# Kernel optimization log

Measured on AMD Instinct MI355X. Metric: run time of the kernel, lower is better.

The kernel has to match this reference:

```python
import jax, jax.numpy as jnp
import numpy as np
import math

B, T, D = 2, 2048, 2048
N_HEADS, N_KV, HEAD_DIM = 16, 4, 128
INTER = 8192
MAX_POS = 4096
ROPE_BASE = 10000.0
EPS = 1e-6


def _rope_tables():
    inv_freq = 1.0 / (ROPE_BASE ** (jnp.arange(0, HEAD_DIM, 2, dtype=jnp.float32) / HEAD_DIM))
    t = jnp.arange(MAX_POS, dtype=jnp.float32)
    freqs = jnp.einsum('i,j->ij', t, inv_freq)          # [MAX_POS, HEAD_DIM//2]
    emb = jnp.concatenate([freqs, freqs], axis=-1)      # [MAX_POS, HEAD_DIM]
    return jnp.cos(emb), jnp.sin(emb)


def _apply_rope(x, cos, sin):
    # x: [B,H,T,Dh]; cos/sin: [B,T,Dh] (gathered by position_ids)
    c = cos[:, None, :, :]
    s = sin[:, None, :, :]
    x1 = x[..., ::2]
    x2 = x[..., 1::2]
    x_rot = jnp.stack([-x2, x1], axis=-1).reshape(x.shape)  # interleave(-x2, x1)
    return x * c + x_rot * s


def _rms_norm(x, w):
    var = jnp.mean(x * x, axis=-1, keepdims=True)
    return w * (x * jax.lax.rsqrt(var + EPS))


def setup_inputs() -> dict:
    key = jax.random.key(0)
    ks = jax.random.split(key, 10)
    s = 0.02
    hidden_states = jax.random.normal(ks[0], (B, T, D), dtype=jnp.float32)
    # additive causal mask
    causal = jnp.tril(jnp.ones((T, T), dtype=bool))
    attention_mask = jnp.where(causal, 0.0, -1e9).astype(jnp.float32)[None, None]
    position_ids = jnp.arange(B * T).reshape(B, T)  # values < MAX_POS
    return {
        'hidden_states': hidden_states,
        'attention_mask': attention_mask,
        'position_ids': position_ids,
        'attn_norm_w': jnp.ones((D,), jnp.float32),
        'mlp_norm_w': jnp.ones((D,), jnp.float32),
        'wq': jax.random.normal(ks[1], (D, N_HEADS * HEAD_DIM), jnp.float32) * s,
        'wk': jax.random.normal(ks[2], (D, N_KV * HEAD_DIM), jnp.float32) * s,
        'wv': jax.random.normal(ks[3], (D, N_KV * HEAD_DIM), jnp.float32) * s,
        'wo': jax.random.normal(ks[4], (N_HEADS * HEAD_DIM, D), jnp.float32) * s,
        'gate_w': jax.random.normal(ks[5], (D, D), jnp.float32) * s,
        'gate_b': jnp.zeros((D,), jnp.float32),
        'fc1_w': jax.random.normal(ks[6], (D, INTER), jnp.float32) * s,
        'fc2_w': jax.random.normal(ks[7], (INTER, D), jnp.float32) * s,
    }


def reference(hidden_states, attention_mask, position_ids, attn_norm_w, mlp_norm_w,
              wq, wk, wv, wo, gate_w, gate_b, fc1_w, fc2_w):
    b, t, _ = hidden_states.shape
    residual = hidden_states
    h = _rms_norm(hidden_states, attn_norm_w)

    # elementwise sigmoid output gate: [B,T,D] -> [B,H,T,Dh]
    gate = jax.nn.sigmoid(h @ gate_w + gate_b)
    gate = gate.reshape(b, t, N_HEADS, HEAD_DIM).transpose(0, 2, 1, 3)

    q = (h @ wq).reshape(b, t, N_HEADS, HEAD_DIM).transpose(0, 2, 1, 3)
    k = (h @ wk).reshape(b, t, N_KV, HEAD_DIM).transpose(0, 2, 1, 3)
    v = (h @ wv).reshape(b, t, N_KV, HEAD_DIM).transpose(0, 2, 1, 3)

    cos_t, sin_t = _rope_tables()
    cos = cos_t[position_ids]  # [B,T,Dh]
    sin = sin_t[position_ids]
    q = _apply_rope(q, cos, sin)
    k = _apply_rope(k, cos, sin)

    n_rep = N_HEADS // N_KV
    k = jnp.repeat(k, n_rep, axis=1)  # GQA expand to [B,H,T,Dh]
    v = jnp.repeat(v, n_rep, axis=1)

    scores = jnp.einsum('bhqd,bhkd->bhqk', q, k) / math.sqrt(HEAD_DIM)
    scores = scores + attention_mask
    attn = jax.nn.softmax(scores, axis=-1)
    out = jnp.einsum('bhqk,bhkd->bhqd', attn, v) * gate
    out = out.transpose(0, 2, 1, 3).reshape(b, t, N_HEADS * HEAD_DIM) @ wo

    h = residual + out
    residual = h
    h2 = _rms_norm(h, mlp_norm_w)
    mlp_out = jax.nn.silu(h2 @ fc1_w) @ fc2_w
    return residual + mlp_out
```

## Files before the change

kernel.cpp:

```cpp
#include <hip/hip_runtime.h>
#include <hip/hip_bf16.h>
#include <cstdint>
#include <cstddef>

#define BB 2
#define TT 2048
#define DD 2048
#define NH 16
#define NKV 4
#define HD 128
#define NI 8192
#define MM (BB*TT)

typedef __bf16 bf16x8 __attribute__((ext_vector_type(8)));
typedef float  f32x4  __attribute__((ext_vector_type(4)));

__device__ __forceinline__ void gload_lds16(const void* g, void* l) {
  __builtin_amdgcn_global_load_lds((__attribute__((address_space(1))) void*)g,
                                   (__attribute__((address_space(3))) void*)l,
                                   16, 0, 0);
}

__device__ __forceinline__ int xcd_swizzle(int wg, int nwg) {
  int xcd = wg & 7;
  int l = wg >> 3;
  int q = nwg >> 3, r = nwg & 7;
  return (xcd < r ? xcd * (q + 1) : r * (q + 1) + (xcd - r) * q) + l;
}

__global__ __launch_bounds__(128) void rope_tables_k(float* __restrict__ cosT,
                                                     float* __restrict__ sinT) {
  int pos = blockIdx.x;
  int d = threadIdx.x;
  int f = d & 63;
  float inv = powf(10000.0f, -((float)(2 * f)) / 128.0f);
  float ang = inv * (float)pos;
  cosT[pos * 128 + d] = cosf(ang);
  sinT[pos * 128 + d] = sinf(ang);
}

template <typename TIN>
__global__ __launch_bounds__(256) void transpose_to_bf16_k(const TIN* __restrict__ in,
                                                           __bf16* __restrict__ out,
                                                           int R, int C) {
  __shared__ float t[32][33];
  int c0 = blockIdx.x * 32, r0 = blockIdx.y * 32;
  int tx = threadIdx.x & 31;
  int ty = threadIdx.x >> 5;
#pragma unroll
  for (int i = 0; i < 4; i++) {
    int r = ty + i * 8;
    t[r][tx] = (float)in[(size_t)(r0 + r) * C + c0 + tx];
  }
  __syncthreads();
#pragma unroll
  for (int i = 0; i < 4; i++) {
    int r = ty + i * 8;
    out[(size_t)(c0 + r) * R + r0 + tx] = (__bf16)t[tx][r];
  }
}

__global__ __launch_bounds__(256) void rmsnorm_k(const float* __restrict__ x,
                                                 const float* __restrict__ w,
                                                 __bf16* __restrict__ out) {
  int row = blockIdx.x;
  const float* xr = x + (size_t)row * DD;
  int t = threadIdx.x;
  float4 a = ((const float4*)xr)[2 * t];
  float4 b = ((const float4*)xr)[2 * t + 1];
  float ss = a.x * a.x + a.y * a.y + a.z * a.z + a.w * a.w +
             b.x * b.x + b.y * b.y + b.z * b.z + b.w * b.w;
#pragma unroll
  for (int off = 32; off; off >>= 1) ss += __shfl_xor(ss, off, 64);
  __shared__ float red[4];
  if ((t & 63) == 0) red[t >> 6] = ss;
  __syncthreads();
  float tot = red[0] + red[1] + red[2] + red[3];
  float rs = rsqrtf(tot * (1.0f / DD) + 1e-6f);
  const float4 w1 = ((const float4*)w)[2 * t];
  const float4 w2 = ((const float4*)w)[2 * t + 1];
  bf16x8 ov;
  ov[0] = (__bf16)(a.x * rs * w1.x);
  ov[1] = (__bf16)(a.y * rs * w1.y);
  ov[2] = (__bf16)(a.z * rs * w1.z);
  ov[3] = (__bf16)(a.w * rs * w1.w);
  ov[4] = (__bf16)(b.x * rs * w2.x);
  ov[5] = (__bf16)(b.y * rs * w2.y);
  ov[6] = (__bf16)(b.z * rs * w2.z);
  ov[7] = (__bf16)(b.w * rs * w2.w);
  *(bf16x8*)(out + (size_t)row * DD + t * 8) = ov;
}

enum { EPI_BF16 = 0, EPI_ROPE = 1, EPI_SIG = 2, EPI_RES = 3, EPI_SILU = 4 };

template <int EPI>
__global__ __launch_bounds__(256) void gemm_k(
    const __bf16* __restrict__ A, const __bf16* __restrict__ Bt,
    __bf16* __restrict__ outB, float* __restrict__ outF,
    const float* __restrict__ bias, const float* __restrict__ residual,
    const float* __restrict__ cosT, const float* __restrict__ sinT,
    const int* __restrict__ posids, int N, int K, float oscale) {
  __shared__ __align__(16) __bf16 As[128 * 32];
  __shared__ __align__(16) __bf16 Bs[128 * 32];
  const int tid = threadIdx.x;
  const int lane = tid & 63;
  const int w = tid >> 6;
  const int wm = w >> 1, wn = w & 1;

  const int nwg = gridDim.x * gridDim.y;
  int wg = xcd_swizzle(blockIdx.y * gridDim.x + blockIdx.x, nwg);
  const int bx = wg % gridDim.x, by = wg / gridDim.x;
  const int m0 = by * 128;
  const int n0 = bx * 128;

  const int lr = lane >> 2;
  const int lc = (lane & 3) * 8;
  const __bf16* aSrc = A + (size_t)(m0 + 32 * w + lr) * K + lc;
  const __bf16* bSrc = Bt + (size_t)(n0 + 32 * w + lr) * K + lc;
  __bf16* aDst = &As[w * 1024];
  __bf16* bDst = &Bs[w * 1024];

  f32x4 acc[4][4];
#pragma unroll
  for (int i = 0; i < 4; i++)
#pragma unroll
    for (int j = 0; j < 4; j++) acc[i][j] = (f32x4){0.f, 0.f, 0.f, 0.f};

  const int fr = lane & 15;
  const int fc = (lane >> 4) * 8;

  for (int k0 = 0; k0 < K; k0 += 32) {
    __syncthreads();
    gload_lds16(aSrc + k0, aDst);
    gload_lds16(aSrc + k0 + (size_t)16 * K, aDst + 512);
    gload_lds16(bSrc + k0, bDst);
    gload_lds16(bSrc + k0 + (size_t)16 * K, bDst + 512);
    asm volatile("s_waitcnt vmcnt(0)" ::: "memory");
    __syncthreads();

    bf16x8 af[4], bfg[4];
#pragma unroll
    for (int i = 0; i < 4; i++)
      af[i] = *(const bf16x8*)&As[(wm * 64 + i * 16 + fr) * 32 + fc];
#pragma unroll
    for (int i = 0; i < 4; i++)
      bfg[i] = *(const bf16x8*)&Bs[(wn * 64 + i * 16 + fr) * 32 + fc];
#pragma unroll
    for (int mi = 0; mi < 4; mi++)
#pragma unroll
      for (int ni = 0; ni < 4; ni++)
        acc[mi][ni] =
            __builtin_amdgcn_mfma_f32_16x16x32_bf16(af[mi], bfg[ni], acc[mi][ni], 0, 0, 0);
  }

  const int fg = lane >> 4;
#pragma unroll
  for (int mi = 0; mi < 4; mi++) {
#pragma unroll
    for (int ni = 0; ni < 4; ni++) {
#pragma unroll
      for (int j = 0; j < 4; j++) {
        int row = m0 + wm * 64 + mi * 16 + fg * 4 + j;
        int col = n0 + wn * 64 + ni * 16 + fr;
        float v = acc[mi][ni][j];
        if constexpr (EPI == EPI_BF16) {
          outB[(size_t)row * N + col] = (__bf16)v;
        } else if constexpr (EPI == EPI_ROPE) {
          float vp = __shfl_xor(v, 1, 64);
          int pos = posids[row];
          int d = col & 127;
          float c = cosT[pos * 128 + d];
          float s = sinT[pos * 128 + d];
          float o = (col & 1) ? (v * c + vp * s) : (v * c - vp * s);
          outB[(size_t)row * N + col] = (__bf16)(o * oscale);
        } else if constexpr (EPI == EPI_SIG) {
          float xx = v + bias[col];
          outB[(size_t)row * N + col] = (__bf16)(1.0f / (1.0f + expf(-xx)));
        } else if constexpr (EPI == EPI_RES) {
          outF[(size_t)row * N + col] = v + residual[(size_t)row * N + col];
        } else if constexpr (EPI == EPI_SILU) {
          outB[(size_t)row * N + col] = (__bf16)(v / (1.0f + expf(-v)));
        }
      }
    }
  }
}

__global__ __launch_bounds__(256) void attn_k(const __bf16* __restrict__ Q,
                                              const __bf16* __restrict__ Kb,
                                              const __bf16* __restrict__ Vt,
                                              const __bf16* __restrict__ Gate,
                                              __bf16* __restrict__ Out) {
  __shared__ __align__(16) __bf16 Ks[2][64 * 128];
  __shared__ __align__(16) __bf16 Vs[2][128 * 64];
  __shared__ __align__(16) __bf16 Ps[4][16 * 64];
  const int tid = threadIdx.x;
  const int lane = tid & 63;
  const int w = tid >> 6;
  const int fr = lane & 15;
  const int fg = lane >> 4;

  const int nwg = gridDim.x * gridDim.y;
  int wg = xcd_swizzle(blockIdx.y * gridDim.x + blockIdx.x, nwg);
  const int qb = wg % gridDim.x;
  const int bh = wg / gridDim.x;
  const int q0 = qb * 64;
  const int b = bh >> 4, h = bh & 15;
  const int g = h >> 2;

  const size_t qrow = (size_t)(b * TT + q0 + w * 16 + fr);
  bf16x8 qf[4];
#pragma unroll
  for (int kt = 0; kt < 4; kt++)
    qf[kt] = *(const bf16x8*)&Q[qrow * 2048 + h * 128 + kt * 32 + fg * 8];

  const __bf16* kPtr[4];
  const __bf16* vPtr[4];
#pragma unroll
  for (int i = 0; i < 4; i++) {
    int krow = w * 16 + i * 4 + (lane >> 4);
    int kcol8 = (lane & 15) ^ (krow & 15);
    kPtr[i] = Kb + (size_t)(b * TT + krow) * 512 + g * 128 + kcol8 * 8;
    int dloc = w * 32 + i * 8 + (lane >> 3);
    int kv8 = (lane & 7) ^ (dloc & 7);
    vPtr[i] = Vt + (size_t)(g * 128 + dloc) * (size_t)MM + b * TT + kv8 * 8;
  }

  f32x4 o[8];
#pragma unroll
  for (int i = 0; i < 8; i++) o[i] = (f32x4){0.f, 0.f, 0.f, 0.f};
  float mrow[4] = {-3e38f, -3e38f, -3e38f, -3e38f};
  float lrow[4] = {0.f, 0.f, 0.f, 0.f};

  const int nsteps = qb + 1;

#pragma unroll
  for (int i = 0; i < 4; i++) {
    gload_lds16(kPtr[i], &Ks[0][w * 2048 + i * 512]);
    gload_lds16(vPtr[i], &Vs[0][w * 2048 + i * 512]);
  }
  __syncthreads();

  for (int t = 0; t < nsteps; t++) {
    const int cur = t & 1;
    const int kb = t * 64;
    if (t + 1 < nsteps) {
      const int nb = kb + 64;
#pragma unroll
      for (int i = 0; i < 4; i++) {
        gload_lds16(kPtr[i] + (size_t)nb * 512, &Ks[cur ^ 1][w * 2048 + i * 512]);
        gload_lds16(vPtr[i] + nb, &Vs[cur ^ 1][w * 2048 + i * 512]);
      }
    }

    f32x4 s[4];
#pragma unroll
    for (int nc = 0; nc < 4; nc++) s[nc] = (f32x4){0.f, 0.f, 0.f, 0.f};
#pragma unroll
    for (int nc = 0; nc < 4; nc++)
#pragma unroll
      for (int kt = 0; kt < 4; kt++) {
        bf16x8 kf = *(const bf16x8*)&Ks[cur][(nc * 16 + fr) * 128 + (((kt * 4 + fg) ^ fr) << 3)];
        s[nc] = __builtin_amdgcn_mfma_f32_16x16x32_bf16(qf[kt], kf, s[nc], 0, 0, 0);
      }

    float alpha[4];
#pragma unroll
    for (int j = 0; j < 4; j++) {
      const int qr = q0 + w * 16 + fg * 4 + j;
      float pv[4];
#pragma unroll
      for (int nc = 0; nc < 4; nc++) {
        int kc = kb + nc * 16 + fr;
        float val = s[nc][j];
        if (kc > qr) val = -1e9f;
        pv[nc] = val;
      }
      float tmx = fmaxf(fmaxf(pv[0], pv[1]), fmaxf(pv[2], pv[3]));
      tmx = fmaxf(tmx, __shfl_xor(tmx, 1, 64));
      tmx = fmaxf(tmx, __shfl_xor(tmx, 2, 64));
      tmx = fmaxf(tmx, __shfl_xor(tmx, 4, 64));
      tmx = fmaxf(tmx, __shfl_xor(tmx, 8, 64));
      float mnew = fmaxf(mrow[j], tmx);
      alpha[j] = __expf(mrow[j] - mnew);
      mrow[j] = mnew;
      float rsum = 0.f;
      const int q = fg * 4 + j;
#pragma unroll
      for (int nc = 0; nc < 4; nc++) {
        float e = __expf(pv[nc] - mnew);
        rsum += e;
        Ps[w][q * 64 + (((nc * 2 + (fr >> 3)) ^ (q & 7)) << 3) + (fr & 7)] = (__bf16)e;
      }
      rsum += __shfl_xor(rsum, 1, 64);
      rsum += __shfl_xor(rsum, 2, 64);
      rsum += __shfl_xor(rsum, 4, 64);
      rsum += __shfl_xor(rsum, 8, 64);
      lrow[j] = lrow[j] * alpha[j] + rsum;
    }
#pragma unroll
    for (int nd = 0; nd < 8; nd++)
#pragma unroll
      for (int j = 0; j < 4; j++) o[nd][j] *= alpha[j];

    bf16x8 pa[2];
#pragma unroll
    for (int sl = 0; sl < 2; sl++)
      pa[sl] = *(const bf16x8*)&Ps[w][fr * 64 + (((sl * 4 + fg) ^ (fr & 7)) << 3)];
#pragma unroll
    for (int nd = 0; nd < 8; nd++)
#pragma unroll
      for (int sl = 0; sl < 2; sl++) {
        bf16x8 vf =
            *(const bf16x8*)&Vs[cur][(nd * 16 + fr) * 64 + (((sl * 4 + fg) ^ (fr & 7)) << 3)];
        o[nd] = __builtin_amdgcn_mfma_f32_16x16x32_bf16(pa[sl], vf, o[nd], 0, 0, 0);
      }
    __syncthreads();
  }

  float invl[4];
#pragma unroll
  for (int j = 0; j < 4; j++) invl[j] = 1.0f / lrow[j];
#pragma unroll
  for (int nd = 0; nd < 8; nd++) {
#pragma unroll
    for (int j = 0; j < 4; j++) {
      int row = q0 + w * 16 + fg * 4 + j;
      int d = nd * 16 + fr;
      size_t idx = (size_t)(b * TT + row) * 2048 + h * 128 + d;
      float val = o[nd][j] * invl[j] * (float)Gate[idx];
      Out[idx] = (__bf16)val;
    }
  }
}

extern "C" void kernel_launch(void* const* d_in, const int* in_sizes, int n_in,
                              void* d_out, int out_size, void* d_ws, size_t ws_size,
                              hipStream_t stream) {
  const float* hidden = (const float*)d_in[0];
  const int* posids = (const int*)d_in[2];
  const float* attn_w = (const float*)d_in[3];
  const float* mlp_w = (const float*)d_in[4];
  const float* wq = (const float*)d_in[5];
  const float* wk = (const float*)d_in[6];
  const float* wv = (const float*)d_in[7];
  const float* wo = (const float*)d_in[8];
  const float* gw = (const float*)d_in[9];
  const float* gb = (const float*)d_in[10];
  const float* f1 = (const float*)d_in[11];
  const float* f2 = (const float*)d_in[12];

  char* p = (char*)d_ws;
  auto alloc = [&](size_t n) {
    char* r = p;
    p += (n + 255) & ~(size_t)255;
    return r;
  };
  __bf16* wq_t = (__bf16*)alloc((size_t)2048 * 2048 * 2);
  __bf16* wk_t = (__bf16*)alloc((size_t)512 * 2048 * 2);
  __bf16* wv_t = (__bf16*)alloc((size_t)512 * 2048 * 2);
  __bf16* gw_t = (__bf16*)alloc((size_t)2048 * 2048 * 2);
  __bf16* wo_t = (__bf16*)alloc((size_t)2048 * 2048 * 2);
  __bf16* f1_t = (__bf16*)alloc((size_t)NI * 2048 * 2);
  __bf16* f2_t = (__bf16*)alloc((size_t)2048 * NI * 2);
  __bf16* h_bf = (__bf16*)alloc((size_t)MM * DD * 2);
  float* h1 = (float*)alloc((size_t)MM * 2048 * 4);

  char* regionA = alloc((size_t)64 * 1024 * 1024);
  __bf16* q_bf    = (__bf16*)(regionA);
  __bf16* gate_bf = (__bf16*)(regionA + (size_t)16 * 1024 * 1024);
  __bf16* attn_g  = (__bf16*)(regionA + (size_t)32 * 1024 * 1024);
  __bf16* k_bf    = (__bf16*)(regionA + (size_t)48 * 1024 * 1024);
  __bf16* v_bf    = (__bf16*)(regionA + (size_t)52 * 1024 * 1024);
  __bf16* v_t     = (__bf16*)(regionA + (size_t)56 * 1024 * 1024);
  float*  cosT    = (float*)(regionA + (size_t)60 * 1024 * 1024);
  float*  sinT    = (float*)(regionA + (size_t)62 * 1024 * 1024);
  __bf16* mlp1    = (__bf16*)(regionA);

  rope_tables_k<<<4096, 128, 0, stream>>>(cosT, sinT);

  transpose_to_bf16_k<float><<<dim3(2048 / 32, 2048 / 32), 256, 0, stream>>>(wq, wq_t, 2048, 2048);
  transpose_to_bf16_k<float><<<dim3(512 / 32, 2048 / 32), 256, 0, stream>>>(wk, wk_t, 2048, 512);
  transpose_to_bf16_k<float><<<dim3(512 / 32, 2048 / 32), 256, 0, stream>>>(wv, wv_t, 2048, 512);
  transpose_to_bf16_k<float><<<dim3(2048 / 32, 2048 / 32), 256, 0, stream>>>(gw, gw_t, 2048, 2048);
  transpose_to_bf16_k<float><<<dim3(2048 / 32, 2048 / 32), 256, 0, stream>>>(wo, wo_t, 2048, 2048);
  transpose_to_bf16_k<float><<<dim3(NI / 32, 2048 / 32), 256, 0, stream>>>(f1, f1_t, 2048, NI);
  transpose_to_bf16_k<float><<<dim3(2048 / 32, NI / 32), 256, 0, stream>>>(f2, f2_t, NI, 2048);

  rmsnorm_k<<<MM, 256, 0, stream>>>(hidden, attn_w, h_bf);

  const float qsc = 0.08838834764831845f;
  gemm_k<EPI_ROPE><<<dim3(16, 32), 256, 0, stream>>>(h_bf, wq_t, q_bf, nullptr, nullptr,
                                                     nullptr, cosT, sinT, posids, 2048, 2048, qsc);
  gemm_k<EPI_ROPE><<<dim3(4, 32), 256, 0, stream>>>(h_bf, wk_t, k_bf, nullptr, nullptr,
                                                    nullptr, cosT, sinT, posids, 512, 2048, 1.0f);
  gemm_k<EPI_BF16><<<dim3(4, 32), 256, 0, stream>>>(h_bf, wv_t, v_bf, nullptr, nullptr,
                                                    nullptr, nullptr, nullptr, nullptr, 512, 2048, 1.0f);
  gemm_k<EPI_SIG><<<dim3(16, 32), 256, 0, stream>>>(h_bf, gw_t, gate_bf, nullptr, gb,
                                                    nullptr, nullptr, nullptr, nullptr, 2048, 2048, 1.0f);

  transpose_to_bf16_k<__bf16><<<dim3(512 / 32, MM / 32), 256, 0, stream>>>(v_bf, v_t, MM, 512);

  attn_k<<<dim3(TT / 64, BB * NH), 256, 0, stream>>>(q_bf, k_bf, v_t, gate_bf, attn_g);

  gemm_k<EPI_RES><<<dim3(16, 32), 256, 0, stream>>>(attn_g, wo_t, nullptr, h1, nullptr,
                                                    hidden, nullptr, nullptr, nullptr, 2048, 2048, 1.0f);

  rmsnorm_k<<<MM, 256, 0, stream>>>(h1, mlp_w, h_bf);

  gemm_k<EPI_SILU><<<dim3(NI / 128, 32), 256, 0, stream>>>(h_bf, f1_t, mlp1, nullptr, nullptr,
                                                           nullptr, nullptr, nullptr, nullptr, NI, 2048, 1.0f);

  gemm_k<EPI_RES><<<dim3(16, 32), 256, 0, stream>>>(mlp1, f2_t, nullptr, (float*)d_out, nullptr,
                                                    h1, nullptr, nullptr, nullptr, 2048, NI, 1.0f);
}
```

Measured before the change: 904.3 us.

## Use 256x256 triple-buffered GEMM, fuse Q/gate and K/V projections, split-K fc2

Replaces the 128x128 GEMM with a 256x256-tile, 512-thread kernel. It uses three-stage LDS buffering with async global-to-LDS loads, XOR-swizzled LDS layout and raised priority around the MFMA block. The Q and gate weights are concatenated into one GEMM, and K and V into another, so each launch shares the same activation loads. The fc2 GEMM is split into two K halves, written as bf16 partials into the reused f1 weight buffer and summed with the residual in a combine kernel. This is meant to raise arithmetic intensity and cut launch count. In exchange it adds bf16 rounding of the partial sums and a larger LDS and register footprint that can lower occupancy.

Result: no change. 904.3 us (+0.0%).

```diff
diff --git a/kernel.cpp b/kernel.cpp
--- a/kernel.cpp
+++ b/kernel.cpp
@@ -91,15 +91,158 @@
   *(bf16x8*)(out + (size_t)row * DD + t * 8) = ov;
 }
 
-enum { EPI_BF16 = 0, EPI_ROPE = 1, EPI_SIG = 2, EPI_RES = 3, EPI_SILU = 4 };
+enum { G_QG = 0, G_RES = 1, G_SILU = 2, G_PART = 3 };
 
 template <int EPI>
-__global__ __launch_bounds__(256) void gemm_k(
+__global__ __launch_bounds__(512) void gemm256_k(
     const __bf16* __restrict__ A, const __bf16* __restrict__ Bt,
     __bf16* __restrict__ outB, float* __restrict__ outF,
+    __bf16* __restrict__ outQ, __bf16* __restrict__ outG,
     const float* __restrict__ bias, const float* __restrict__ residual,
     const float* __restrict__ cosT, const float* __restrict__ sinT,
-    const int* __restrict__ posids, int N, int K, float oscale) {
+    const int* __restrict__ posids, int N, int K, int ldk, float oscale) {
+  __shared__ __align__(16) __bf16 Ab[3][256 * 32];
+  __shared__ __align__(16) __bf16 Bb[3][256 * 32];
+  const int tid = threadIdx.x;
+  const int lane = tid & 63;
+  const int wid = tid >> 6;
+  const int wr = wid >> 2;
+  const int wc = wid & 3;
+  const int fr = lane & 15;
+  const int fg = lane >> 4;
+
+  const int nwg = gridDim.x * gridDim.y;
+  int wg = xcd_swizzle(blockIdx.y * gridDim.x + blockIdx.x, nwg);
+  const int bx = wg % gridDim.x, by = wg / gridDim.x;
+  const int m0 = by * 256;
+  const int n0 = bx * 256;
+  const int kz = blockIdx.z;
+  const int kBase = kz * K;
+
+  const int srow0 = wid * 32 + (lane >> 2);
+  const int scol = (((lane & 3) ^ ((lane >> 3) & 3)) << 3);
+  const __bf16* aS0 = A + (size_t)(m0 + srow0) * ldk + kBase + scol;
+  const __bf16* aS1 = aS0 + (size_t)16 * ldk;
+  const __bf16* bS0 = Bt + (size_t)(n0 + srow0) * ldk + kBase + scol;
+  const __bf16* bS1 = bS0 + (size_t)16 * ldk;
+  const int e0 = (wid * 2) * 512;
+  const int e1 = (wid * 2 + 1) * 512;
+
+  const int nt = K / 32;
+
+#define STAGE256(kt, s)                             \
+  {                                                 \
+    const int k0_ = (kt) * 32;                      \
+    gload_lds16(aS0 + k0_, &Ab[(s)][e0]);           \
+    gload_lds16(aS1 + k0_, &Ab[(s)][e1]);           \
+    gload_lds16(bS0 + k0_, &Bb[(s)][e0]);           \
+    gload_lds16(bS1 + k0_, &Bb[(s)][e1]);           \
+  }
+
+  STAGE256(0, 0);
+  if (nt > 1) STAGE256(1, 1);
+  asm volatile("s_waitcnt vmcnt(4)" ::: "memory");
+  __builtin_amdgcn_s_barrier();
+  __builtin_amdgcn_sched_barrier(0);
+
+  f32x4 acc[8][4];
+#pragma unroll
+  for (int i = 0; i < 8; i++)
+#pragma unroll
+    for (int j = 0; j < 4; j++) acc[i][j] = (f32x4){0.f, 0.f, 0.f, 0.f};
+
+  const int asl = (fg ^ ((fr >> 1) & 3)) * 8;
+
+  for (int t = 0; t < nt; ++t) {
+    const int s = t % 3;
+    if (t + 2 < nt) STAGE256(t + 2, (t + 2) % 3);
+    bf16x8 af[8], bfr[4];
+#pragma unroll
+    for (int mi = 0; mi < 8; mi++)
+      af[mi] = *(const bf16x8*)&Ab[s][(wr * 128 + mi * 16 + fr) * 32 + asl];
+#pragma unroll
+    for (int ni = 0; ni < 4; ni++)
+      bfr[ni] = *(const bf16x8*)&Bb[s][(wc * 64 + ni * 16 + fr) * 32 + asl];
+    __builtin_amdgcn_s_setprio(1);
+#pragma unroll
+    for (int mi = 0; mi < 8; mi++)
+#pragma unroll
+      for (int ni = 0; ni < 4; ni++)
+        acc[mi][ni] =
+            __builtin_amdgcn_mfma_f32_16x16x32_bf16(af[mi], bfr[ni], acc[mi][ni], 0, 0, 0);
+    __builtin_amdgcn_s_setprio(0);
+    if (t + 1 < nt) {
+      if (t + 2 < nt) {
+        asm volatile("s_waitcnt vmcnt(4)" ::: "memory");
+      } else {
+        asm volatile("s_waitcnt vmcnt(0)" ::: "memory");
+      }
+      __builtin_amdgcn_s_barrier();
+      __builtin_amdgcn_sched_barrier(0);
+    }
+  }
+#undef STAGE256
+
+#pragma unroll
+  for (int mi = 0; mi < 8; mi++) {
+    const int row = m0 + wr * 128 + mi * 16 + fg * 4;
+#pragma unroll
+    for (int ni = 0; ni < 4; ni++) {
+      const int col = n0 + wc * 64 + ni * 16 + fr;
+#pragma unroll
+      for (int j = 0; j < 4; j++) {
+        float v = acc[mi][ni][j];
+        const int r = row + j;
+        if constexpr (EPI == G_QG) {
+          float vp = __shfl_xor(v, 1, 64);
+          if (n0 < 2048) {
+            int pos = posids[r];
+            int d = col & 127;
+            float c = cosT[pos * 128 + d], sn = sinT[pos * 128 + d];
+            float o = (col & 1) ? (v * c + vp * sn) : (v * c - vp * sn);
+            outQ[(size_t)r * 2048 + col] = (__bf16)(o * oscale);
+          } else {
+            float xx = v + bias[col - 2048];
+            outG[(size_t)r * 2048 + (col - 2048)] = (__bf16)(1.0f / (1.0f + expf(-xx)));
+          }
+        } else if constexpr (EPI == G_RES) {
+          outF[(size_t)r * N + col] = v + residual[(size_t)r * N + col];
+        } else if constexpr (EPI == G_SILU) {
+          outB[(size_t)r * N + col] = (__bf16)(v / (1.0f + expf(-v)));
+        } else {
+          outB[(size_t)(kz * MM + r) * N + col] = (__bf16)v;
+        }
+      }
+    }
+  }
+}
+
+__global__ __launch_bounds__(256) void combine_k(const __bf16* __restrict__ parts,
+                                                 const float* __restrict__ h1,
+                                                 float* __restrict__ out) {
+  size_t i = ((size_t)blockIdx.x * 256 + threadIdx.x) * 8;
+  bf16x8 p0 = *(const bf16x8*)&parts[i];
+  bf16x8 p1 = *(const bf16x8*)&parts[(size_t)MM * 2048 + i];
+  float4 a = *(const float4*)&h1[i];
+  float4 b = *(const float4*)&h1[i + 4];
+  float4 o0, o1;
+  o0.x = (float)p0[0] + (float)p1[0] + a.x;
+  o0.y = (float)p0[1] + (float)p1[1] + a.y;
+  o0.z = (float)p0[2] + (float)p1[2] + a.z;
+  o0.w = (float)p0[3] + (float)p1[3] + a.w;
+  o1.x = (float)p0[4] + (float)p1[4] + b.x;
+  o1.y = (float)p0[5] + (float)p1[5] + b.y;
+  o1.z = (float)p0[6] + (float)p1[6] + b.z;
+  o1.w = (float)p0[7] + (float)p1[7] + b.w;
+  *(float4*)&out[i] = o0;
+  *(float4*)&out[i + 4] = o1;
+}
+
+__global__ __launch_bounds__(256) void gemm_kv_k(
+    const __bf16* __restrict__ A, const __bf16* __restrict__ Bt,
+    __bf16* __restrict__ kOut, __bf16* __restrict__ vOut,
+    const float* __restrict__ cosT, const float* __restrict__ sinT,
+    const int* __restrict__ posids, int K) {
   __shared__ __align__(16) __bf16 As[128 * 32];
   __shared__ __align__(16) __bf16 Bs[128 * 32];
   const int tid = threadIdx.x;
@@ -163,23 +306,16 @@
         int row = m0 + wm * 64 + mi * 16 + fg * 4 + j;
         int col = n0 + wn * 64 + ni * 16 + fr;
         float v = acc[mi][ni][j];
-        if constexpr (EPI == EPI_BF16) {
-          outB[(size_t)row * N + col] = (__bf16)v;
-        } else if constexpr (EPI == EPI_ROPE) {
-          float vp = __shfl_xor(v, 1, 64);
+        float vp = __shfl_xor(v, 1, 64);
+        if (col < 512) {
           int pos = posids[row];
           int d = col & 127;
           float c = cosT[pos * 128 + d];
           float s = sinT[pos * 128 + d];
           float o = (col & 1) ? (v * c + vp * s) : (v * c - vp * s);
-          outB[(size_t)row * N + col] = (__bf16)(o * oscale);
-        } else if constexpr (EPI == EPI_SIG) {
-          float xx = v + bias[col];
-          outB[(size_t)row * N + col] = (__bf16)(1.0f / (1.0f + expf(-xx)));
-        } else if constexpr (EPI == EPI_RES) {
-          outF[(size_t)row * N + col] = v + residual[(size_t)row * N + col];
-        } else if constexpr (EPI == EPI_SILU) {
-          outB[(size_t)row * N + col] = (__bf16)(v / (1.0f + expf(-v)));
+          kOut[(size_t)row * 512 + col] = (__bf16)o;
+        } else {
+          vOut[(size_t)row * 512 + (col - 512)] = (__bf16)v;
         }
       }
     }
@@ -356,10 +492,8 @@
     p += (n + 255) & ~(size_t)255;
     return r;
   };
-  __bf16* wq_t = (__bf16*)alloc((size_t)2048 * 2048 * 2);
-  __bf16* wk_t = (__bf16*)alloc((size_t)512 * 2048 * 2);
-  __bf16* wv_t = (__bf16*)alloc((size_t)512 * 2048 * 2);
-  __bf16* gw_t = (__bf16*)alloc((size_t)2048 * 2048 * 2);
+  __bf16* wqg_t = (__bf16*)alloc((size_t)4096 * 2048 * 2);
+  __bf16* wkv_t = (__bf16*)alloc((size_t)1024 * 2048 * 2);
   __bf16* wo_t = (__bf16*)alloc((size_t)2048 * 2048 * 2);
   __bf16* f1_t = (__bf16*)alloc((size_t)NI * 2048 * 2);
   __bf16* f2_t = (__bf16*)alloc((size_t)2048 * NI * 2);
@@ -367,50 +501,52 @@
   float* h1 = (float*)alloc((size_t)MM * 2048 * 4);
 
   char* regionA = alloc((size_t)64 * 1024 * 1024);
-  __bf16* q_bf    = (__bf16*)(regionA);
+  __bf16* q_bf = (__bf16*)(regionA);
   __bf16* gate_bf = (__bf16*)(regionA + (size_t)16 * 1024 * 1024);
-  __bf16* attn_g  = (__bf16*)(regionA + (size_t)32 * 1024 * 1024);
-  __bf16* k_bf    = (__bf16*)(regionA + (size_t)48 * 1024 * 1024);
-  __bf16* v_bf    = (__bf16*)(regionA + (size_t)52 * 1024 * 1024);
-  __bf16* v_t     = (__bf16*)(regionA + (size_t)56 * 1024 * 1024);
-  float*  cosT    = (float*)(regionA + (size_t)60 * 1024 * 1024);
-  float*  sinT    = (float*)(regionA + (size_t)62 * 1024 * 1024);
-  __bf16* mlp1    = (__bf16*)(regionA);
+  __bf16* attn_g = (__bf16*)(regionA + (size_t)32 * 1024 * 1024);
+  __bf16* k_bf = (__bf16*)(regionA + (size_t)48 * 1024 * 1024);
+  __bf16* v_bf = (__bf16*)(regionA + (size_t)52 * 1024 * 1024);
+  __bf16* v_t = (__bf16*)(regionA + (size_t)56 * 1024 * 1024);
+  float* cosT = (float*)(regionA + (size_t)60 * 1024 * 1024);
+  float* sinT = (float*)(regionA + (size_t)62 * 1024 * 1024);
+  __bf16* mlp1 = (__bf16*)(regionA);
+  __bf16* parts = (__bf16*)f1_t;
 
   rope_tables_k<<<4096, 128, 0, stream>>>(cosT, sinT);
 
-  transpose_to_bf16_k<float><<<dim3(2048 / 32, 2048 / 32), 256, 0, stream>>>(wq, wq_t, 2048, 2048);
-  transpose_to_bf16_k<float><<<dim3(512 / 32, 2048 / 32), 256, 0, stream>>>(wk, wk_t, 2048, 512);
-  transpose_to_bf16_k<float><<<dim3(512 / 32, 2048 / 32), 256, 0, stream>>>(wv, wv_t, 2048, 512);
-  transpose_to_bf16_k<float><<<dim3(2048 / 32, 2048 / 32), 256, 0, stream>>>(gw, gw_t, 2048, 2048);
-  transpose_to_bf16_k<float><<<dim3(2048 / 32, 2048 / 32), 256, 0, stream>>>(wo, wo_t, 2048, 2048);
-  transpose_to_bf16_k<float><<<dim3(NI / 32, 2048 / 32), 256, 0, stream>>>(f1, f1_t, 2048, NI);
-  transpose_to_bf16_k<float><<<dim3(2048 / 32, NI / 32), 256, 0, stream>>>(f2, f2_t, NI, 2048);
+  transpose_to_bf16_k<float><<<dim3(64, 64), 256, 0, stream>>>(wq, wqg_t, 2048, 2048);
+  transpose_to_bf16_k<float><<<dim3(64, 64), 256, 0, stream>>>(gw, wqg_t + (size_t)2048 * 2048, 2048, 2048);
+  transpose_to_bf16_k<float><<<dim3(16, 64), 256, 0, stream>>>(wk, wkv_t, 2048, 512);
+  transpose_to_bf16_k<float><<<dim3(16, 64), 256, 0, stream>>>(wv, wkv_t + (size_t)512 * 2048, 2048, 512);
+  transpose_to_bf16_k<float><<<dim3(64, 64), 256, 0, stream>>>(wo, wo_t, 2048, 2048);
+  transpose_to_bf16_k<float><<<dim3(256, 64), 256, 0, stream>>>(f1, f1_t, 2048, NI);
+  transpose_to_bf16_k<float><<<dim3(64, 256), 256, 0, stream>>>(f2, f2_t, NI, 2048);
 
   rmsnorm_k<<<MM, 256, 0, stream>>>(hidden, attn_w, h_bf);
 
   const float qsc = 0.08838834764831845f;
-  gemm_k<EPI_ROPE><<<dim3(16, 32), 256, 0, stream>>>(h_bf, wq_t, q_bf, nullptr, nullptr,
-                                                     nullptr, cosT, sinT, posids, 2048, 2048, qsc);
-  gemm_k<EPI_ROPE><<<dim3(4, 32), 256, 0, stream>>>(h_bf, wk_t, k_bf, nullptr, nullptr,
-                                                    nullptr, cosT, sinT, posids, 512, 2048, 1.0f);
-  gemm_k<EPI_BF16><<<dim3(4, 32), 256, 0, stream>>>(h_bf, wv_t, v_bf, nullptr, nullptr,
-                                                    nullptr, nullptr, nullptr, nullptr, 512, 2048, 1.0f);
-  gemm_k<EPI_SIG><<<dim3(16, 32), 256, 0, stream>>>(h_bf, gw_t, gate_bf, nullptr, gb,
-                                                    nullptr, nullptr, nullptr, nullptr, 2048, 2048, 1.0f);
-
-  transpose_to_bf16_k<__bf16><<<dim3(512 / 32, MM / 32), 256, 0, stream>>>(v_bf, v_t, MM, 512);
-
-  attn_k<<<dim3(TT / 64, BB * NH), 256, 0, stream>>>(q_bf, k_bf, v_t, gate_bf, attn_g);
-
-  gemm_k<EPI_RES><<<dim3(16, 32), 256, 0, stream>>>(attn_g, wo_t, nullptr, h1, nullptr,
-                                                    hidden, nullptr, nullptr, nullptr, 2048, 2048, 1.0f);
+  gemm256_k<G_QG><<<dim3(16, 16), 512, 0, stream>>>(
+      h_bf, wqg_t, nullptr, nullptr, q_bf, gate_bf, gb, nullptr, cosT, sinT, posids,
+      4096, 2048, 2048, qsc);
+  gemm_kv_k<<<dim3(8, 32), 256, 0, stream>>>(h_bf, wkv_t, k_bf, v_bf, cosT, sinT, posids, 2048);
+
+  transpose_to_bf16_k<__bf16><<<dim3(16, 128), 256, 0, stream>>>(v_bf, v_t, MM, 512);
+
+  attn_k<<<dim3(32, 32), 256, 0, stream>>>(q_bf, k_bf, v_t, gate_bf, attn_g);
+
+  gemm256_k<G_RES><<<dim3(8, 16), 512, 0, stream>>>(
+      attn_g, wo_t, nullptr, h1, nullptr, nullptr, nullptr, hidden, nullptr, nullptr, nullptr,
+      2048, 2048, 2048, 1.0f);
 
   rmsnorm_k<<<MM, 256, 0, stream>>>(h1, mlp_w, h_bf);
 
-  gemm_k<EPI_SILU><<<dim3(NI / 128, 32), 256, 0, stream>>>(h_bf, f1_t, mlp1, nullptr, nullptr,
-                                                           nullptr, nullptr, nullptr, nullptr, NI, 2048, 1.0f);
-
-  gemm_k<EPI_RES><<<dim3(16, 32), 256, 0, stream>>>(mlp1, f2_t, nullptr, (float*)d_out, nullptr,
-                                                    h1, nullptr, nullptr, nullptr, 2048, NI, 1.0f);
-}
+  gemm256_k<G_SILU><<<dim3(32, 16), 512, 0, stream>>>(
+      h_bf, f1_t, mlp1, nullptr, nullptr, nullptr, nullptr, nullptr, nullptr, nullptr, nullptr,
+      NI, 2048, 2048, 1.0f);
+
+  gemm256_k<G_PART><<<dim3(8, 16, 2), 512, 0, stream>>>(
+      mlp1, f2_t, parts, nullptr, nullptr, nullptr, nullptr, nullptr, nullptr, nullptr, nullptr,
+      2048, 4096, NI, 1.0f);
+
+  combine_k<<<4096, 256, 0, stream>>>(parts, h1, (float*)d_out);
+}
```
